# Kernel tuning notes

Measured on AMD Instinct MI355X. Metric: run time of the kernel, lower is better.

## Reference

```python
import jax, jax.numpy as jnp
import numpy as np

S_SRC, S_TGT, N = 50, 50, 64
E, H, V_SRC, V_TGT = 300, 512, 10000, 10000


def setup_inputs() -> dict:
    key = jax.random.key(0)
    ks = jax.random.split(key, 20)
    p = lambda k, shape: jax.random.normal(k, shape, dtype=jnp.float32) * 0.02
    inp = {
        'source': jax.random.randint(ks[0], (S_SRC, N), 0, V_SRC),
        'target': jax.random.randint(ks[1], (S_TGT, N), 0, V_TGT),
        'enc_emb': p(ks[2], (V_SRC, E)),
        'enc_Wih_f': p(ks[3], (4 * H, E)),
        'enc_Whh_f': p(ks[4], (4 * H, H)),
        'enc_b_f': jnp.zeros((4 * H,), jnp.float32),
        'enc_Wih_b': p(ks[5], (4 * H, E)),
        'enc_Whh_b': p(ks[6], (4 * H, H)),
        'enc_b_b': jnp.zeros((4 * H,), jnp.float32),
        'fc_hid_W': p(ks[7], (H, 2 * H)),
        'fc_hid_b': jnp.zeros((H,), jnp.float32),
        'fc_cell_W': p(ks[8], (H, 2 * H)),
        'fc_cell_b': jnp.zeros((H,), jnp.float32),
        'dec_emb': p(ks[9], (V_TGT, E)),
        'dec_Wih': p(ks[10], (4 * H, 2 * H + E)),
        'dec_Whh': p(ks[11], (4 * H, H)),
        'dec_b': jnp.zeros((4 * H,), jnp.float32),
        'energy_W': p(ks[12], (1, 3 * H)),
        'energy_b': jnp.zeros((1,), jnp.float32),
        'fc_W': p(ks[13], (V_TGT, H)),
        'fc_b': jnp.zeros((V_TGT,), jnp.float32),
    }
    return inp


def lstm_cell(x, h, c, Wih, Whh, b):
    # x:[N,Din] h,c:[N,H]  PyTorch gate order: i,f,g,o
    gates = x @ Wih.T + h @ Whh.T + b
    i, f, g, o = jnp.split(gates, 4, axis=-1)
    i, f, o = jax.nn.sigmoid(i), jax.nn.sigmoid(f), jax.nn.sigmoid(o)
    c_new = f * c + i * jnp.tanh(g)
    h_new = o * jnp.tanh(c_new)
    return h_new, c_new


def _forward(source, target, enc_emb, enc_Wih_f, enc_Whh_f, enc_b_f,
             enc_Wih_b, enc_Whh_b, enc_b_b, fc_hid_W, fc_hid_b,
             fc_cell_W, fc_cell_b, dec_emb, dec_Wih, dec_Whh, dec_b,
             energy_W, energy_b, fc_W, fc_b):
    emb = enc_emb[source]  # [S,N,E]  (dropout = identity, eval)
    h0 = jnp.zeros((source.shape[1], H), jnp.float32)

    def fwd_step(carry, x_t):
        h, c = carry
        h, c = lstm_cell(x_t, h, c, enc_Wih_f, enc_Whh_f, enc_b_f)
        return (h, c), h

    def bwd_step(carry, x_t):
        h, c = carry
        h, c = lstm_cell(x_t, h, c, enc_Wih_b, enc_Whh_b, enc_b_b)
        return (h, c), h

    (hf, cf), out_f = jax.lax.scan(fwd_step, (h0, h0), emb)
    (hb, cb), out_b = jax.lax.scan(bwd_step, (h0, h0), emb[::-1])
    encoder_states = jnp.concatenate([out_f, out_b[::-1]], axis=-1)  # [S,N,2H]

    hidden = jnp.concatenate([hf, hb], axis=-1) @ fc_hid_W.T + fc_hid_b  # [N,H]
    cell = jnp.concatenate([cf, cb], axis=-1) @ fc_cell_W.T + fc_cell_b

    def dec_step(carry, x_t):
        h, c = carry
        e = dec_emb[x_t]  # [N,E]
        # energy: Linear(cat(hidden_repeat[S,N,H], enc_states[S,N,2H])) -> [S,N,1]
        Wh, We = energy_W[:, :H], energy_W[:, H:]  # split avoids materializing concat
        energy = jax.nn.relu(h @ Wh.T + jnp.einsum('snl,kl->snk', encoder_states, We) + energy_b)
        attn = jax.nn.softmax(energy, axis=0)  # softmax over seq dim
        context = jnp.einsum('sn,snl->nl', attn[..., 0], encoder_states)  # [N,2H]
        rnn_in = jnp.concatenate([context, e], axis=-1)  # [N,2H+E]
        h, c = lstm_cell(rnn_in, h, c, dec_Wih, dec_Whh, dec_b)
        pred = h @ fc_W.T + fc_b  # [N,V]
        return (h, c), pred

    # teacher_force_ratio=1.0: inputs are target[0..T-2]
    _, preds = jax.lax.scan(dec_step, (hidden, cell), target[:-1])
    zeros0 = jnp.zeros((1,) + preds.shape[1:], preds.dtype)
    return jnp.concatenate([zeros0, preds], axis=0)  # [T,N,V], row 0 zeros


def reference(source, target, enc_emb, enc_Wih_f, enc_Whh_f, enc_b_f,
              enc_Wih_b, enc_Whh_b, enc_b_b, fc_hid_W, fc_hid_b,
              fc_cell_W, fc_cell_b, dec_emb, dec_Wih, dec_Whh, dec_b,
              energy_W, energy_b, fc_W, fc_b):
    return _forward(source, target, enc_emb, enc_Wih_f, enc_Whh_f, enc_b_f,
                    enc_Wih_b, enc_Whh_b, enc_b_b, fc_hid_W, fc_hid_b,
                    fc_cell_W, fc_cell_b, dec_emb, dec_Wih, dec_Whh, dec_b,
                    energy_W, energy_b, fc_W, fc_b)
```

## Files before the change

kernel.cpp:

```cpp
#include <hip/hip_runtime.h>
#include <math.h>

#define SSRC 50
#define NBATCH 64
#define EDIM 300
#define HDIM 512
#define G4H 2048
#define VTGT 10000
#define TSTEPS 49

#define HS4 8192

__device__ __forceinline__ float ld1_agent(const float* p) {
    return __hip_atomic_load(p, __ATOMIC_RELAXED, __HIP_MEMORY_SCOPE_AGENT);
}
__device__ __forceinline__ void st1_agent(float* p, float v) {
    __hip_atomic_store(p, v, __ATOMIC_RELAXED, __HIP_MEMORY_SCOPE_AGENT);
}
__device__ __forceinline__ float2 ld2_agent(const float* p) {
    unsigned long long u = __hip_atomic_load((const unsigned long long*)p,
                                             __ATOMIC_RELAXED, __HIP_MEMORY_SCOPE_AGENT);
    union { unsigned long long u; float2 f; } c; c.u = u; return c.f;
}
__device__ __forceinline__ void st2_agent(float* p, float x, float y) {
    union { float2 f; unsigned long long u; } c; c.f.x = x; c.f.y = y;
    __hip_atomic_store((unsigned long long*)p, c.u, __ATOMIC_RELAXED, __HIP_MEMORY_SCOPE_AGENT);
}

__device__ __forceinline__ void gbar(int* cnt, int nblk, int& gen)
{
    asm volatile("s_waitcnt vmcnt(0)" ::: "memory");
    __syncthreads();
    if (threadIdx.x == 0) {
        __hip_atomic_fetch_add(cnt, 1, __ATOMIC_RELAXED, __HIP_MEMORY_SCOPE_AGENT);
        gen += nblk;
        const long long t0 = (long long)__builtin_amdgcn_s_memrealtime();
        while (__hip_atomic_load(cnt, __ATOMIC_RELAXED, __HIP_MEMORY_SCOPE_AGENT) < gen) {
            __builtin_amdgcn_s_sleep(2);
            if ((long long)__builtin_amdgcn_s_memrealtime() - t0 > 200000000LL) break;
        }
    }
    __syncthreads();
}

__device__ __forceinline__ int gswz(int kk, int c) {
    return kk * 128 + ((c ^ (((c >> 6) & 1) << 2)) ^ (kk << 2));
}

__global__ __launch_bounds__(256)
void gemm_bias_kernel(const float* __restrict__ A, const int* __restrict__ aidx, int lda,
                      const float* __restrict__ B, int ldb,
                      const float* __restrict__ bias,
                      float* __restrict__ C, int ldc,
                      int M, int N, int K, int a_trans)
{
    __shared__ float As[8 * 128];
    __shared__ float Bs[8 * 128];
    const int tid = threadIdx.x;
    const int bm = blockIdx.y * 128;
    const int bn = blockIdx.x * 128;
    const int tx = tid & 15;
    const int ty = tid >> 4;

    float acc[8][8];
#pragma unroll
    for (int i = 0; i < 8; ++i)
#pragma unroll
        for (int j = 0; j < 8; ++j) acc[i][j] = 0.f;

    for (int k0 = 0; k0 < K; k0 += 8) {
#pragma unroll
        for (int i = 0; i < 4; ++i) {
            int idx = tid + i * 256;
            {
                int r, kk;
                if (a_trans) { r = idx & 127; kk = idx >> 7; }
                else         { r = idx >> 3; kk = idx & 7; }
                int gm = bm + r, gk = k0 + kk;
                float va = 0.f;
                if (gm < M && gk < K) {
                    if (a_trans) va = A[(long)gk * lda + gm];
                    else {
                        long arow = aidx ? (long)aidx[gm] : (long)gm;
                        va = A[arow * (long)lda + gk];
                    }
                }
                As[gswz(kk, r)] = va;
            }
            {
                int r = idx >> 3, kk = idx & 7;
                int gn = bn + r, gk = k0 + kk;
                float vb = 0.f;
                if (gn < N && gk < K) vb = B[(long)gn * ldb + gk];
                Bs[gswz(kk, r)] = vb;
            }
        }
        __syncthreads();
#pragma unroll
        for (int kk = 0; kk < 8; ++kk) {
            const float4 a0 = *reinterpret_cast<const float4*>(&As[gswz(kk, ty * 8)]);
            const float4 a1 = *reinterpret_cast<const float4*>(&As[gswz(kk, ty * 8 + 4)]);
            const float4 b0 = *reinterpret_cast<const float4*>(&Bs[gswz(kk, tx * 8)]);
            const float4 b1 = *reinterpret_cast<const float4*>(&Bs[gswz(kk, tx * 8 + 4)]);
            const float a[8] = {a0.x, a0.y, a0.z, a0.w, a1.x, a1.y, a1.z, a1.w};
            const float b[8] = {b0.x, b0.y, b0.z, b0.w, b1.x, b1.y, b1.z, b1.w};
#pragma unroll
            for (int i = 0; i < 8; ++i)
#pragma unroll
                for (int j = 0; j < 8; ++j)
                    acc[i][j] = fmaf(a[i], b[j], acc[i][j]);
        }
        __syncthreads();
    }

#pragma unroll
    for (int i = 0; i < 8; ++i) {
        int m = bm + ty * 8 + i;
        if (m >= M) continue;
#pragma unroll
        for (int j = 0; j < 8; ++j) {
            int n = bn + tx * 8 + j;
            if (n >= N) continue;
            float v = acc[i][j];
            if (bias) v += bias[n];
            C[(long)m * ldc + n] = v;
        }
    }
}

__global__ __launch_bounds__(256)
void enc_wt_kernel(const float* __restrict__ Wf, const float* __restrict__ Wb,
                   float4* __restrict__ Wt)
{
    const int F = blockIdx.x * 256 + threadIdx.x;
    if (F >= 2 * 16 * 128 * 128) return;
    const int jj = F & 127;
    const int l4 = (F >> 7) & 127;
    const int r  = F >> 14;
    const int dir = r >> 4, jg = r & 15;
    const int jglob = (jj & 3) * 512 + jg * 32 + (jj >> 2);
    const float* src = dir ? Wb : Wf;
    Wt[F] = *reinterpret_cast<const float4*>(src + (size_t)jglob * 512 + l4 * 4);
}

__global__ __launch_bounds__(256)
void dec_wt_kernel(const float* __restrict__ Wih, const float* __restrict__ Whh,
                   float4* __restrict__ Wt)
{
    const int F = blockIdx.x * 256 + threadIdx.x;
    if (F >= 32 * 384 * 64) return;
    const int j = F & 63;
    const int t = F >> 6;
    const int l4 = t % 384, jg = t / 384;
    const int jglob = (j & 3) * 512 + jg * 16 + (j >> 2);
    const int l = l4 * 4;
    float4 v;
    if (l < 1024) v = *reinterpret_cast<const float4*>(Wih + (size_t)jglob * 1324 + l);
    else          v = *reinterpret_cast<const float4*>(Whh + (size_t)jglob * 512 + (l - 1024));
    Wt[F] = v;
}

struct EncArgs {
    const float* Xf; const float* Xb;
    const float4* WtE;
    float* hT;
    float* cT;
    float* catSt;
    const float* energy_W; const float* energy_b;
    float* eeT;
    const float* fc_hid_W; const float* fc_hid_b;
    const float* fc_cell_W; const float* fc_cell_b;
    float* dhT;
    float* dcT;
    int* bars;
};

__global__ __launch_bounds__(1024)
void enc_persistent(EncArgs a)
{
    __shared__ float actL[8 * 516];
    __shared__ float red[8 * 8 * 128];
    const int blk = blockIdx.x;
    const int tid = threadIdx.x;
    const int lane = tid & 63;
    const int w    = tid >> 6;
    const int lc   = w >> 1;
    const int jh   = w & 1;
    const int dir  = blk >> 7;
    const int db   = blk & 127;
    const int jg   = (db & 7) * 2 + (db >> 6);
    const int ng   = (db >> 3) & 7;
    int genD = 0, genF = 0;

    const float* X   = dir ? a.Xb : a.Xf;
    float* hTd  = a.hT + (size_t)dir * 2 * 4 * HS4;
    float* cTd  = a.cT + (size_t)dir * 4 * HS4;
    const float4* Wt = a.WtE + (size_t)(dir * 16 + jg) * 128 * 128;

    const int pw_n  = ng * 8 + (tid >> 5);
    const int pw_kl = tid & 31;
    const int pw_k  = jg * 32 + pw_kl;
    const int pw_ci = (pw_k >> 2) * 256 + pw_n * 4 + (pw_k & 3);
    float c_reg = 0.f;

    for (int t = 0; t < SSRC; ++t) {
        const int xoff = dir ? (SSRC - 1 - t) : t;
        const float* hbase = hTd + (size_t)(t & 1) * 4 * HS4;
        float xg0 = 0.f, xg1 = 0.f, xg2 = 0.f, xg3 = 0.f;
        if (tid < 256) {
            const float* Xr = X + (size_t)xoff * (NBATCH * G4H) + pw_n * G4H + pw_k;
            xg0 = __builtin_nontemporal_load(Xr);
            xg1 = __builtin_nontemporal_load(Xr + 512);
            xg2 = __builtin_nontemporal_load(Xr + 1024);
            xg3 = __builtin_nontemporal_load(Xr + 1536);
        }
        {
            const int nh = tid & 7, l4g = tid >> 3;
            const float* hp = hbase + ((size_t)l4g * 64 + ng * 8 + nh) * 4;
            const float2 lo = ld2_agent(hp), hi = ld2_agent(hp + 2);
            float4 v; v.x = lo.x; v.y = lo.y; v.z = hi.x; v.w = hi.y;
            *reinterpret_cast<float4*>(&actL[nh * 516 + l4g * 4]) = v;
        }
        __syncthreads();
        float acc[8];
#pragma unroll
        for (int q = 0; q < 8; ++q) acc[q] = 0.f;
        {
            const float4* wp = Wt + (size_t)(lc * 16) * 128 + jh * 64 + lane;
            for (int i = 0; i < 16; ++i) {
                const float4 wv = wp[(size_t)i * 128];
                const int l4 = lc * 16 + i;
#pragma unroll
                for (int q = 0; q < 8; ++q) {
                    const float4 av = *reinterpret_cast<const float4*>(&actL[q * 516 + l4 * 4]);
                    acc[q] = fmaf(av.w, wv.w, fmaf(av.z, wv.z,
                              fmaf(av.y, wv.y, fmaf(av.x, wv.x, acc[q]))));
                }
            }
        }
#pragma unroll
        for (int q = 0; q < 8; ++q) red[lc * 1024 + q * 128 + jh * 64 + lane] = acc[q];
        __syncthreads();
        if (tid < 256) {
            const int nh = tid >> 5;
            float g0 = xg0, g1 = xg1, g2 = xg2, g3 = xg3;
#pragma unroll
            for (int l2 = 0; l2 < 8; ++l2) {
                const float* rp = &red[l2 * 1024 + nh * 128 + pw_kl * 4];
                g0 += rp[0]; g1 += rp[1]; g2 += rp[2]; g3 += rp[3];
            }
            const float si = 1.f / (1.f + __expf(-g0));
            const float sf = 1.f / (1.f + __expf(-g1));
            const float so = 1.f / (1.f + __expf(-g3));
            const float tg = tanhf(g2);
            c_reg = sf * c_reg + si * tg;
            const float hn = so * tanhf(c_reg);
            st1_agent(&(hTd + (size_t)((t + 1) & 1) * 4 * HS4)[pw_ci], hn);
            st1_agent(&a.catSt[((size_t)xoff * 64 + pw_n) * 1024 + dir * 512 + pw_k], hn);
            if (t == SSRC - 1) st1_agent(&cTd[pw_ci], c_reg);
        }
        gbar(a.bars + dir, 128, genD);
    }
    gbar(a.bars + 2, 256, genF);

    const int n = lane;
    if (blk < SSRC) {
        const int s = blk;
        const int nl = tid & 63, ch = tid >> 6;
        const float* row = a.catSt + ((size_t)s * 64 + nl) * 1024;
        const float* We = a.energy_W + 512;
        float p = 0.f;
        for (int l4 = ch * 16; l4 < ch * 16 + 16; ++l4) {
            const float2 s01 = ld2_agent(row + l4 * 4);
            const float2 s23 = ld2_agent(row + l4 * 4 + 2);
            const float4 wv = *reinterpret_cast<const float4*>(We + l4 * 4);
            p += s01.x * wv.x + s01.y * wv.y + s23.x * wv.z + s23.y * wv.w;
        }
        red[ch * 64 + nl] = p;
        __syncthreads();
        if (ch == 0) {
            float sum = a.energy_b[0];
#pragma unroll
            for (int q = 0; q < 16; ++q) sum += red[q * 64 + nl];
            a.eeT[s * 64 + nl] = sum;
        }
    } else if (blk >= 64 && blk < 192) {
        const bool cell = blk >= 128;
        const int kb2 = (blk & 63) * 8;
        const float* W   = cell ? a.fc_cell_W : a.fc_hid_W;
        const float* bs  = cell ? a.fc_cell_b : a.fc_hid_b;
        const float* Afl = cell ? a.cT : a.hT;
        const float* Abl = cell ? (a.cT + (size_t)4 * HS4) : (a.hT + (size_t)8 * HS4);
        const int kl2 = w >> 1, lh = w & 1;
        const int k = kb2 + kl2;
        const float* Wr = W + (size_t)k * 1024;
        float acc = 0.f;
        for (int l4 = lh * 64; l4 < lh * 64 + 64; ++l4) {
            const float* pA = Afl + ((size_t)l4 * 64 + n) * 4;
            const float2 u01 = ld2_agent(pA), u23 = ld2_agent(pA + 2);
            const float4 wv = *reinterpret_cast<const float4*>(Wr + l4 * 4);
            acc += u01.x * wv.x + u01.y * wv.y + u23.x * wv.z + u23.y * wv.w;
            const float* pB = Abl + ((size_t)l4 * 64 + n) * 4;
            const float2 v01 = ld2_agent(pB), v23 = ld2_agent(pB + 2);
            const float4 wv2 = *reinterpret_cast<const float4*>(Wr + 512 + l4 * 4);
            acc += v01.x * wv2.x + v01.y * wv2.y + v23.x * wv2.z + v23.y * wv2.w;
        }
        red[(kl2 * 2 + lh) * 64 + n] = acc;
        __syncthreads();
        if (w < 8) {
            const float v = bs[kb2 + w] + red[(w * 2) * 64 + n] + red[(w * 2 + 1) * 64 + n];
            const int k2 = kb2 + w;
            const int ci = (k2 >> 2) * 256 + n * 4 + (k2 & 3);
            (cell ? a.dcT : a.dhT)[ci] = v;
        }
    }
}

struct DecArgs {
    const float* Xd;
    const float4* WtD;
    const float* Wh;
    const float* eeT;
    const float* catSt;
    float* dhT;
    const float* dcT;
    float* ctxG;
    float* HsT;
    int* bar;
};

__global__ __launch_bounds__(1024)
void dec_persistent(DecArgs a)
{
    __shared__ float  actL[8][1544];
    __shared__ float  red[16 * 544];
    __shared__ float4 cpart[16][64];
    __shared__ float  WhL[512];
    __shared__ float  eeL[SSRC * 8];
    __shared__ float  attnL[SSRC * 8];
    __shared__ float  hdl[8];
    const int blk = blockIdx.x;
    const int tid = threadIdx.x;
    const int lane = tid & 63;
    const int w    = tid >> 6;
    const int jg   = (blk & 7) * 4 + (blk >> 6);
    const int ng   = (blk >> 3) & 7;
    int gen = 0;
    const float4* Wt = a.WtD + (size_t)jg * 384 * 64;

    if (tid < 512) WhL[tid] = a.Wh[tid];
    if (tid < SSRC * 8) eeL[tid] = a.eeT[(tid >> 3) * 64 + ng * 8 + (tid & 7)];
    __syncthreads();

    const int pw_kl = tid >> 3, pw_nh = tid & 7;
    const int pw_k = jg * 16 + pw_kl;
    const int pw_n = ng * 8 + pw_nh;
    const int pw_ci = (pw_k >> 2) * 256 + pw_n * 4 + (pw_k & 3);
    float c_reg = 0.f;
    if (tid < 128) c_reg = ld1_agent(&a.dcT[pw_ci]);

    for (int t = 0; t < TSTEPS; ++t) {
        const float* hc = a.dhT + (size_t)(t & 1) * 32768;
        float xg0 = 0.f, xg1 = 0.f, xg2 = 0.f, xg3 = 0.f;
        if (tid < 128) {
            const float* Xr = a.Xd + (size_t)t * (NBATCH * G4H) + pw_n * G4H + pw_k;
            xg0 = __builtin_nontemporal_load(Xr);
            xg1 = __builtin_nontemporal_load(Xr + 512);
            xg2 = __builtin_nontemporal_load(Xr + 1024);
            xg3 = __builtin_nontemporal_load(Xr + 1536);
        }
        {
            const int nh = tid & 7, l4g = tid >> 3;
            const float* hp = hc + ((size_t)l4g * 64 + ng * 8 + nh) * 4;
            const float2 lo = ld2_agent(hp), hi = ld2_agent(hp + 2);
            float4 v; v.x = lo.x; v.y = lo.y; v.z = hi.x; v.w = hi.y;
            *reinterpret_cast<float4*>(&actL[nh][1024 + l4g * 4]) = v;
        }
        __syncthreads();
        if (w < 8) {
            const float4 h0 = *reinterpret_cast<const float4*>(&actL[w][1024 + lane * 4]);
            const float4 h1 = *reinterpret_cast<const float4*>(&actL[w][1024 + (lane + 64) * 4]);
            const float4 w0 = *reinterpret_cast<const float4*>(&WhL[lane * 4]);
            const float4 w1 = *reinterpret_cast<const float4*>(&WhL[(lane + 64) * 4]);
            float p = h0.x * w0.x + h0.y * w0.y + h0.z * w0.z + h0.w * w0.w
                    + h1.x * w1.x + h1.y * w1.y + h1.z * w1.z + h1.w * w1.w;
#pragma unroll
            for (int off = 32; off > 0; off >>= 1) p += __shfl_down(p, off);
            if (lane == 0) hdl[w] = p;
        }
        __syncthreads();
        if (tid < 8) {
            const float hd = hdl[tid];
            float m = 0.f;
            for (int s = 0; s < SSRC; ++s) m = fmaxf(m, hd + eeL[s * 8 + tid]);
            float ssum = 0.f;
            for (int s = 0; s < SSRC; ++s) {
                float e = hd + eeL[s * 8 + tid];
                e = e > 0.f ? e : 0.f;
                const float ex = __expf(e - m);
                attnL[s * 8 + tid] = ex;
                ssum += ex;
            }
            const float inv = 1.f / ssum;
            for (int s = 0; s < SSRC; ++s) attnL[s * 8 + tid] *= inv;
        }
        __syncthreads();
        {
            const int sh = tid >> 6, nc = tid & 63;
            const int nh = nc >> 3, c = nc & 7;
            const float* sp = a.catSt + ((size_t)ng * 8 + nh) * 1024 + jg * 32 + c * 4;
            float4 acc4{0.f, 0.f, 0.f, 0.f};
            for (int s = sh; s < SSRC; s += 16) {
                const float aw = attnL[s * 8 + nh];
                const float* q = sp + (size_t)s * 64 * 1024;
                const float2 lo = ld2_agent(q), hi = ld2_agent(q + 2);
                acc4.x = fmaf(aw, lo.x, acc4.x);
                acc4.y = fmaf(aw, lo.y, acc4.y);
                acc4.z = fmaf(aw, hi.x, acc4.z);
                acc4.w = fmaf(aw, hi.y, acc4.w);
            }
            cpart[sh][nc] = acc4;
        }
        __syncthreads();
        if (tid < 64) {
            const int nh = tid >> 3, c = tid & 7;
            float4 s4{0.f, 0.f, 0.f, 0.f};
#pragma unroll
            for (int sh = 0; sh < 16; ++sh) {
                const float4 v = cpart[sh][tid];
                s4.x += v.x; s4.y += v.y; s4.z += v.z; s4.w += v.w;
            }
            float* cp = a.ctxG + ((size_t)ng * 8 + nh) * 1024 + jg * 32 + c * 4;
            st2_agent(cp, s4.x, s4.y);
            st2_agent(cp + 2, s4.z, s4.w);
        }
        gbar(a.bar, 256, gen);
#pragma unroll
        for (int i = 0; i < 2; ++i) {
            const int e = tid + i * 1024;
            const int l4g = e & 255, nh = e >> 8;
            const float* cp = a.ctxG + ((size_t)ng * 8 + nh) * 1024 + l4g * 4;
            const float2 lo = ld2_agent(cp), hi = ld2_agent(cp + 2);
            float4 v; v.x = lo.x; v.y = lo.y; v.z = hi.x; v.w = hi.y;
            *reinterpret_cast<float4*>(&actL[nh][l4g * 4]) = v;
        }
        __syncthreads();
        float acc[8];
#pragma unroll
        for (int q = 0; q < 8; ++q) acc[q] = 0.f;
        {
            const float4* wp = Wt + (size_t)(w * 24) * 64 + lane;
            for (int i = 0; i < 24; ++i) {
                const float4 wv = wp[(size_t)i * 64];
                const int l4 = w * 24 + i;
#pragma unroll
                for (int q = 0; q < 8; ++q) {
                    const float4 av = *reinterpret_cast<const float4*>(&actL[q][l4 * 4]);
                    acc[q] = fmaf(av.w, wv.w, fmaf(av.z, wv.z,
                              fmaf(av.y, wv.y, fmaf(av.x, wv.x, acc[q]))));
                }
            }
        }
#pragma unroll
        for (int q = 0; q < 8; ++q) red[w * 544 + q * 68 + lane] = acc[q];
        __syncthreads();
        if (tid < 128) {
            float g4[4];
#pragma unroll
            for (int g = 0; g < 4; ++g) {
                const int j = pw_kl * 4 + g;
                float v = 0.f;
#pragma unroll
                for (int w2 = 0; w2 < 16; ++w2) v += red[w2 * 544 + pw_nh * 68 + j];
                g4[g] = v;
            }
            g4[0] += xg0; g4[1] += xg1; g4[2] += xg2; g4[3] += xg3;
            const float si = 1.f / (1.f + __expf(-g4[0]));
            const float sf = 1.f / (1.f + __expf(-g4[1]));
            const float so = 1.f / (1.f + __expf(-g4[3]));
            const float tg = tanhf(g4[2]);
            c_reg = sf * c_reg + si * tg;
            const float hn = so * tanhf(c_reg);
            st1_agent(&(a.dhT + (size_t)((t + 1) & 1) * 32768)[pw_ci], hn);
            st1_agent(&a.HsT[(size_t)pw_k * (TSTEPS * NBATCH) + t * 64 + pw_n], hn);
        }
        gbar(a.bar, 256, gen);
    }
}

extern "C" void kernel_launch(void* const* d_in, const int* in_sizes, int n_in,
                              void* d_out, int out_size, void* d_ws, size_t ws_size,
                              hipStream_t stream)
{
    const int*   source    = (const int*)  d_in[0];
    const int*   target    = (const int*)  d_in[1];
    const float* enc_emb   = (const float*)d_in[2];
    const float* enc_Wih_f = (const float*)d_in[3];
    const float* enc_Whh_f = (const float*)d_in[4];
    const float* enc_b_f   = (const float*)d_in[5];
    const float* enc_Wih_b = (const float*)d_in[6];
    const float* enc_Whh_b = (const float*)d_in[7];
    const float* enc_b_b   = (const float*)d_in[8];
    const float* fc_hid_W  = (const float*)d_in[9];
    const float* fc_hid_b  = (const float*)d_in[10];
    const float* fc_cell_W = (const float*)d_in[11];
    const float* fc_cell_b = (const float*)d_in[12];
    const float* dec_emb   = (const float*)d_in[13];
    const float* dec_Wih   = (const float*)d_in[14];
    const float* dec_Whh   = (const float*)d_in[15];
    const float* dec_b     = (const float*)d_in[16];
    const float* energy_W  = (const float*)d_in[17];
    const float* energy_b  = (const float*)d_in[18];
    const float* fc_W      = (const float*)d_in[19];
    const float* fc_b      = (const float*)d_in[20];
    float* out = (float*)d_out;

    float* w = (float*)d_ws;
    size_t o = 0;
    auto alloc = [&](size_t nf) { float* p = w + o; o += nf; return p; };
    const size_t HS = (size_t)NBATCH * HDIM;
    float* Xf    = alloc((size_t)SSRC * NBATCH * G4H);
    float* Xb    = alloc((size_t)SSRC * NBATCH * G4H);
    float* catSt = alloc((size_t)SSRC * NBATCH * 1024);
    float* hT    = alloc(4 * HS);
    float* cT    = alloc(2 * HS);
    float* dhT   = alloc(2 * HS);
    float* dcT   = alloc(1 * HS);
    float* eeT   = alloc((size_t)SSRC * NBATCH);
    float* HsT   = alloc((size_t)HDIM * TSTEPS * NBATCH);
    float* WtE   = alloc((size_t)2 * 16 * 128 * 512);
    int*   bars  = (int*)alloc(16);
    float* Xd    = Xf;
    float* ctxG  = hT;
    float* WtD   = Xb;

    hipMemsetAsync(hT, 0, 4 * HS * sizeof(float), stream);
    hipMemsetAsync(bars, 0, 16 * sizeof(int), stream);
    hipMemsetAsync(out, 0, (size_t)NBATCH * VTGT * sizeof(float), stream);

    {
        dim3 g(G4H / 128, (SSRC * NBATCH + 127) / 128);
        gemm_bias_kernel<<<g, 256, 0, stream>>>(enc_emb, source, EDIM, enc_Wih_f, EDIM,
                                                enc_b_f, Xf, G4H, SSRC * NBATCH, G4H, EDIM, 0);
        gemm_bias_kernel<<<g, 256, 0, stream>>>(enc_emb, source, EDIM, enc_Wih_b, EDIM,
                                                enc_b_b, Xb, G4H, SSRC * NBATCH, G4H, EDIM, 0);
    }
    enc_wt_kernel<<<(2 * 16 * 128 * 128 + 255) / 256, 256, 0, stream>>>(
        enc_Whh_f, enc_Whh_b, (float4*)WtE);

    {
        EncArgs ea{Xf, Xb, (const float4*)WtE, hT, cT, catSt,
                   energy_W, energy_b, eeT, fc_hid_W, fc_hid_b, fc_cell_W, fc_cell_b,
                   dhT, dcT, bars};
        enc_persistent<<<256, 1024, 0, stream>>>(ea);
    }

    {
        dim3 g(G4H / 128, (TSTEPS * NBATCH + 127) / 128);
        gemm_bias_kernel<<<g, 256, 0, stream>>>(dec_emb, target, EDIM, dec_Wih + 2 * HDIM,
                                                2 * HDIM + EDIM, dec_b, Xd, G4H,
                                                TSTEPS * NBATCH, G4H, EDIM, 0);
    }
    dec_wt_kernel<<<(32 * 384 * 64 + 255) / 256, 256, 0, stream>>>(
        dec_Wih, dec_Whh, (float4*)WtD);

    {
        DecArgs da{Xd, (const float4*)WtD, energy_W, eeT, catSt,
                   dhT, dcT, ctxG, HsT, bars + 3};
        dec_persistent<<<256, 1024, 0, stream>>>(da);
    }

    {
        dim3 g((VTGT + 127) / 128, (TSTEPS * NBATCH + 127) / 128);
        gemm_bias_kernel<<<g, 256, 0, stream>>>(HsT, nullptr, TSTEPS * NBATCH, fc_W, HDIM,
                                                fc_b, out + (size_t)NBATCH * VTGT, VTGT,
                                                TSTEPS * NBATCH, VTGT, HDIM, 1);
    }
}
```

Before: 3.800 ms.

## Precompute attention-context gate projection and remove mid-step grid barrier in decoder

Uses linearity to precompute Wih_ctx · encoder_states for every source position (a GEMM over all 50 positions before the decoder). The per-step context term then becomes an attention-weighted sum of these precomputed gate contributions, which removes the ctxG exchange and one grid barrier per step and shrinks the recurrent matvec to the Whh part only. The attention dot product h·Wh is also computed as per-block partials written at the end of the previous step. The trade-off is a large up-front GEMM plus extra reads of G4 each step.

```diff
diff --git a/kernel.cpp b/kernel.cpp
--- a/kernel.cpp
+++ b/kernel.cpp
@@ -21,10 +21,6 @@
     unsigned long long u = __hip_atomic_load((const unsigned long long*)p,
                                              __ATOMIC_RELAXED, __HIP_MEMORY_SCOPE_AGENT);
     union { unsigned long long u; float2 f; } c; c.u = u; return c.f;
-}
-__device__ __forceinline__ void st2_agent(float* p, float x, float y) {
-    union { float2 f; unsigned long long u; } c; c.f.x = x; c.f.y = y;
-    __hip_atomic_store((unsigned long long*)p, c.u, __ATOMIC_RELAXED, __HIP_MEMORY_SCOPE_AGENT);
 }
 
 __device__ __forceinline__ void gbar(int* cnt, int nblk, int& gen)
@@ -52,7 +48,7 @@
                       const float* __restrict__ B, int ldb,
                       const float* __restrict__ bias,
                       float* __restrict__ C, int ldc,
-                      int M, int N, int K, int a_trans)
+                      int M, int N, int K, int a_trans, int c_mode)
 {
     __shared__ float As[8 * 128];
     __shared__ float Bs[8 * 128];
@@ -123,7 +119,13 @@
             if (n >= N) continue;
             float v = acc[i][j];
             if (bias) v += bias[n];
-            C[(long)m * ldc + n] = v;
+            if (c_mode == 0) {
+                C[(long)m * ldc + n] = v;
+            } else {
+                const int jg = m >> 6, jl = m & 63;
+                const int s = n >> 6, ng = (n >> 3) & 7, nl = n & 7;
+                C[(size_t)(((jg * 8 + ng) * 50 + s) * 512) + jl * 8 + nl] = v;
+            }
         }
     }
 }
@@ -144,20 +146,23 @@
 }
 
 __global__ __launch_bounds__(256)
-void dec_wt_kernel(const float* __restrict__ Wih, const float* __restrict__ Whh,
-                   float4* __restrict__ Wt)
+void dec_wt3_kernel(const float* __restrict__ Whh, float4* __restrict__ Wt)
 {
     const int F = blockIdx.x * 256 + threadIdx.x;
-    if (F >= 32 * 384 * 64) return;
-    const int j = F & 63;
-    const int t = F >> 6;
-    const int l4 = t % 384, jg = t / 384;
+    if (F >= 32 * 128 * 64) return;
+    const int j  = F & 63;
+    const int l4 = (F >> 6) & 127;
+    const int jg = F >> 13;
     const int jglob = (j & 3) * 512 + jg * 16 + (j >> 2);
-    const int l = l4 * 4;
-    float4 v;
-    if (l < 1024) v = *reinterpret_cast<const float4*>(Wih + (size_t)jglob * 1324 + l);
-    else          v = *reinterpret_cast<const float4*>(Whh + (size_t)jglob * 512 + (l - 1024));
-    Wt[F] = v;
+    Wt[F] = *reinterpret_cast<const float4*>(Whh + (size_t)jglob * 512 + l4 * 4);
+}
+
+__global__ __launch_bounds__(256)
+void aidx_kernel(int* __restrict__ aidx)
+{
+    const int m = blockIdx.x * 256 + threadIdx.x;
+    if (m >= 2048) return;
+    aidx[m] = (m & 3) * 512 + (m >> 6) * 16 + ((m >> 2) & 15);
 }
 
 struct EncArgs {
@@ -318,13 +323,13 @@
 
 struct DecArgs {
     const float* Xd;
-    const float4* WtD;
+    const float4* Wt3;
+    const float* G4;
     const float* Wh;
     const float* eeT;
-    const float* catSt;
     float* dhT;
     const float* dcT;
-    float* ctxG;
+    float* hdP;
     float* HsT;
     int* bar;
 };
@@ -332,24 +337,27 @@
 __global__ __launch_bounds__(1024)
 void dec_persistent(DecArgs a)
 {
-    __shared__ float  actL[8][1544];
+    __shared__ float  actL[8][520];
     __shared__ float  red[16 * 544];
-    __shared__ float4 cpart[16][64];
+    __shared__ float4 red3[8][64][2];
     __shared__ float  WhL[512];
-    __shared__ float  eeL[SSRC * 8];
-    __shared__ float  attnL[SSRC * 8];
+    __shared__ float  eeL[SSRC][9];
+    __shared__ float  attnL[SSRC][8];
     __shared__ float  hdl[8];
+    __shared__ float  hdpl[32][8];
+    __shared__ float  hdkl[16][8];
     const int blk = blockIdx.x;
     const int tid = threadIdx.x;
-    const int lane = tid & 63;
-    const int w    = tid >> 6;
-    const int jg   = (blk & 7) * 4 + (blk >> 6);
-    const int ng   = (blk >> 3) & 7;
+    const int lane = tid & 63, w = tid >> 6;
+    const int jg = (blk & 7) * 4 + ((blk >> 3) & 3);
+    const int ng = blk >> 5;
     int gen = 0;
-    const float4* Wt = a.WtD + (size_t)jg * 384 * 64;
+    const float4* Wt = a.Wt3 + (size_t)jg * 128 * 64;
+    const float*  Gt = a.G4 + (size_t)(jg * 8 + ng) * 50 * 512;
 
     if (tid < 512) WhL[tid] = a.Wh[tid];
-    if (tid < SSRC * 8) eeL[tid] = a.eeT[(tid >> 3) * 64 + ng * 8 + (tid & 7)];
+    if (tid < SSRC * 8)
+        eeL[tid >> 3][tid & 7] = a.eeT[(tid >> 3) * 64 + ng * 8 + (tid & 7)];
     __syncthreads();
 
     const int pw_kl = tid >> 3, pw_nh = tid & 7;
@@ -361,6 +369,13 @@
 
     for (int t = 0; t < TSTEPS; ++t) {
         const float* hc = a.dhT + (size_t)(t & 1) * 32768;
+        {
+            const int nh = tid & 7, l4g = tid >> 3;
+            const float* hp = hc + ((size_t)l4g * 64 + ng * 8 + nh) * 4;
+            const float2 lo = ld2_agent(hp), hi = ld2_agent(hp + 2);
+            float4 v; v.x = lo.x; v.y = lo.y; v.z = hi.x; v.w = hi.y;
+            *reinterpret_cast<float4*>(&actL[nh][l4g * 4]) = v;
+        }
         float xg0 = 0.f, xg1 = 0.f, xg2 = 0.f, xg3 = 0.f;
         if (tid < 128) {
             const float* Xr = a.Xd + (size_t)t * (NBATCH * G4H) + pw_n * G4H + pw_k;
@@ -369,112 +384,95 @@
             xg2 = __builtin_nontemporal_load(Xr + 1024);
             xg3 = __builtin_nontemporal_load(Xr + 1536);
         }
+        __syncthreads();
+        if (t == 0) {
+            if (w < 8) {
+                const float4 h0 = *reinterpret_cast<const float4*>(&actL[w][lane * 4]);
+                const float4 h1 = *reinterpret_cast<const float4*>(&actL[w][(lane + 64) * 4]);
+                const float4 w0 = *reinterpret_cast<const float4*>(&WhL[lane * 4]);
+                const float4 w1 = *reinterpret_cast<const float4*>(&WhL[(lane + 64) * 4]);
+                float p = h0.x * w0.x + h0.y * w0.y + h0.z * w0.z + h0.w * w0.w
+                        + h1.x * w1.x + h1.y * w1.y + h1.z * w1.z + h1.w * w1.w;
+#pragma unroll
+                for (int off = 32; off > 0; off >>= 1) p += __shfl_down(p, off);
+                if (lane == 0) hdl[w] = p;
+            }
+        } else {
+            if (tid < 256) {
+                const int q = tid >> 3, nh = tid & 7;
+                hdpl[q][nh] = ld1_agent(&a.hdP[q * 64 + ng * 8 + nh]);
+            }
+            __syncthreads();
+            if (tid < 8) {
+                float s = 0.f;
+#pragma unroll
+                for (int q = 0; q < 32; ++q) s += hdpl[q][tid];
+                hdl[tid] = s;
+            }
+        }
+        __syncthreads();
+        if (w < 8) {
+            const float hd = hdl[w];
+            float e = 0.f;
+            if (lane < SSRC) { e = hd + eeL[lane][w]; e = e > 0.f ? e : 0.f; }
+            float m = e;
+#pragma unroll
+            for (int off = 32; off > 0; off >>= 1) m = fmaxf(m, __shfl_xor(m, off));
+            float ex = (lane < SSRC) ? __expf(e - m) : 0.f;
+            float ssum = ex;
+#pragma unroll
+            for (int off = 32; off > 0; off >>= 1) ssum += __shfl_xor(ssum, off);
+            if (lane < SSRC) attnL[lane][w] = ex / ssum;
+        }
+        __syncthreads();
         {
-            const int nh = tid & 7, l4g = tid >> 3;
-            const float* hp = hc + ((size_t)l4g * 64 + ng * 8 + nh) * 4;
-            const float2 lo = ld2_agent(hp), hi = ld2_agent(hp + 2);
-            float4 v; v.x = lo.x; v.y = lo.y; v.z = hi.x; v.w = hi.y;
-            *reinterpret_cast<float4*>(&actL[nh][1024 + l4g * 4]) = v;
-        }
-        __syncthreads();
-        if (w < 8) {
-            const float4 h0 = *reinterpret_cast<const float4*>(&actL[w][1024 + lane * 4]);
-            const float4 h1 = *reinterpret_cast<const float4*>(&actL[w][1024 + (lane + 64) * 4]);
-            const float4 w0 = *reinterpret_cast<const float4*>(&WhL[lane * 4]);
-            const float4 w1 = *reinterpret_cast<const float4*>(&WhL[(lane + 64) * 4]);
-            float p = h0.x * w0.x + h0.y * w0.y + h0.z * w0.z + h0.w * w0.w
-                    + h1.x * w1.x + h1.y * w1.y + h1.z * w1.z + h1.w * w1.w;
-#pragma unroll
-            for (int off = 32; off > 0; off >>= 1) p += __shfl_down(p, off);
-            if (lane == 0) hdl[w] = p;
-        }
-        __syncthreads();
-        if (tid < 8) {
-            const float hd = hdl[tid];
-            float m = 0.f;
-            for (int s = 0; s < SSRC; ++s) m = fmaxf(m, hd + eeL[s * 8 + tid]);
-            float ssum = 0.f;
-            for (int s = 0; s < SSRC; ++s) {
-                float e = hd + eeL[s * 8 + tid];
-                e = e > 0.f ? e : 0.f;
-                const float ex = __expf(e - m);
-                attnL[s * 8 + tid] = ex;
-                ssum += ex;
-            }
-            const float inv = 1.f / ssum;
-            for (int s = 0; s < SSRC; ++s) attnL[s * 8 + tid] *= inv;
-        }
-        __syncthreads();
+            const int jl = tid & 63, sh = (tid >> 6) & 7, nhh = tid >> 9;
+            const float* Gp = Gt + jl * 8 + nhh * 4;
+            float4 acc4{0.f, 0.f, 0.f, 0.f};
+            for (int s = sh; s < SSRC; s += 8) {
+                const float4 av = *reinterpret_cast<const float4*>(&attnL[s][nhh * 4]);
+                const float4 gv = *reinterpret_cast<const float4*>(Gp + (size_t)s * 512);
+                acc4.x = fmaf(av.x, gv.x, acc4.x);
+                acc4.y = fmaf(av.y, gv.y, acc4.y);
+                acc4.z = fmaf(av.z, gv.z, acc4.z);
+                acc4.w = fmaf(av.w, gv.w, acc4.w);
+            }
+            red3[sh][jl][nhh] = acc4;
+        }
         {
-            const int sh = tid >> 6, nc = tid & 63;
-            const int nh = nc >> 3, c = nc & 7;
-            const float* sp = a.catSt + ((size_t)ng * 8 + nh) * 1024 + jg * 32 + c * 4;
-            float4 acc4{0.f, 0.f, 0.f, 0.f};
-            for (int s = sh; s < SSRC; s += 16) {
-                const float aw = attnL[s * 8 + nh];
-                const float* q = sp + (size_t)s * 64 * 1024;
-                const float2 lo = ld2_agent(q), hi = ld2_agent(q + 2);
-                acc4.x = fmaf(aw, lo.x, acc4.x);
-                acc4.y = fmaf(aw, lo.y, acc4.y);
-                acc4.z = fmaf(aw, hi.x, acc4.z);
-                acc4.w = fmaf(aw, hi.y, acc4.w);
-            }
-            cpart[sh][nc] = acc4;
-        }
-        __syncthreads();
-        if (tid < 64) {
-            const int nh = tid >> 3, c = tid & 7;
-            float4 s4{0.f, 0.f, 0.f, 0.f};
-#pragma unroll
-            for (int sh = 0; sh < 16; ++sh) {
-                const float4 v = cpart[sh][tid];
-                s4.x += v.x; s4.y += v.y; s4.z += v.z; s4.w += v.w;
-            }
-            float* cp = a.ctxG + ((size_t)ng * 8 + nh) * 1024 + jg * 32 + c * 4;
-            st2_agent(cp, s4.x, s4.y);
-            st2_agent(cp + 2, s4.z, s4.w);
-        }
-        gbar(a.bar, 256, gen);
-#pragma unroll
-        for (int i = 0; i < 2; ++i) {
-            const int e = tid + i * 1024;
-            const int l4g = e & 255, nh = e >> 8;
-            const float* cp = a.ctxG + ((size_t)ng * 8 + nh) * 1024 + l4g * 4;
-            const float2 lo = ld2_agent(cp), hi = ld2_agent(cp + 2);
-            float4 v; v.x = lo.x; v.y = lo.y; v.z = hi.x; v.w = hi.y;
-            *reinterpret_cast<float4*>(&actL[nh][l4g * 4]) = v;
-        }
-        __syncthreads();
-        float acc[8];
-#pragma unroll
-        for (int q = 0; q < 8; ++q) acc[q] = 0.f;
-        {
-            const float4* wp = Wt + (size_t)(w * 24) * 64 + lane;
-            for (int i = 0; i < 24; ++i) {
+            float acc2[8];
+#pragma unroll
+            for (int q = 0; q < 8; ++q) acc2[q] = 0.f;
+            const float4* wp = Wt + (size_t)(w * 8) * 64 + lane;
+            for (int i = 0; i < 8; ++i) {
                 const float4 wv = wp[(size_t)i * 64];
-                const int l4 = w * 24 + i;
+                const int l4 = w * 8 + i;
 #pragma unroll
                 for (int q = 0; q < 8; ++q) {
                     const float4 av = *reinterpret_cast<const float4*>(&actL[q][l4 * 4]);
-                    acc[q] = fmaf(av.w, wv.w, fmaf(av.z, wv.z,
-                              fmaf(av.y, wv.y, fmaf(av.x, wv.x, acc[q]))));
+                    acc2[q] = fmaf(av.w, wv.w, fmaf(av.z, wv.z,
+                               fmaf(av.y, wv.y, fmaf(av.x, wv.x, acc2[q]))));
                 }
             }
-        }
-#pragma unroll
-        for (int q = 0; q < 8; ++q) red[w * 544 + q * 68 + lane] = acc[q];
+#pragma unroll
+            for (int q = 0; q < 8; ++q) red[w * 544 + q * 68 + lane] = acc2[q];
+        }
         __syncthreads();
         if (tid < 128) {
-            float g4[4];
+            const float* r3f = reinterpret_cast<const float*>(red3);
+            const int base = pw_nh >> 2, cc = pw_nh & 3;
+            float g4[4] = {xg0, xg1, xg2, xg3};
 #pragma unroll
             for (int g = 0; g < 4; ++g) {
                 const int j = pw_kl * 4 + g;
-                float v = 0.f;
+                float v = g4[g];
 #pragma unroll
                 for (int w2 = 0; w2 < 16; ++w2) v += red[w2 * 544 + pw_nh * 68 + j];
+#pragma unroll
+                for (int sh = 0; sh < 8; ++sh)
+                    v += r3f[(size_t)(sh * 128 + j * 2 + base) * 4 + cc];
                 g4[g] = v;
             }
-            g4[0] += xg0; g4[1] += xg1; g4[2] += xg2; g4[3] += xg3;
             const float si = 1.f / (1.f + __expf(-g4[0]));
             const float sf = 1.f / (1.f + __expf(-g4[1]));
             const float so = 1.f / (1.f + __expf(-g4[3]));
@@ -483,6 +481,14 @@
             const float hn = so * tanhf(c_reg);
             st1_agent(&(a.dhT + (size_t)((t + 1) & 1) * 32768)[pw_ci], hn);
             st1_agent(&a.HsT[(size_t)pw_k * (TSTEPS * NBATCH) + t * 64 + pw_n], hn);
+            hdkl[pw_kl][pw_nh] = WhL[pw_k] * hn;
+        }
+        __syncthreads();
+        if (tid < 8) {
+            float s = 0.f;
+#pragma unroll
+            for (int kl = 0; kl < 16; ++kl) s += hdkl[kl][tid];
+            st1_agent(&a.hdP[jg * 64 + ng * 8 + tid], s);
         }
         gbar(a.bar, 256, gen);
     }
@@ -529,10 +535,12 @@
     float* eeT   = alloc((size_t)SSRC * NBATCH);
     float* HsT   = alloc((size_t)HDIM * TSTEPS * NBATCH);
     float* WtE   = alloc((size_t)2 * 16 * 128 * 512);
+    float* Wt3   = alloc((size_t)32 * 128 * 64 * 4);
+    float* hdP   = alloc((size_t)32 * 64);
+    int*   aidxA = (int*)alloc(2048);
     int*   bars  = (int*)alloc(16);
     float* Xd    = Xf;
-    float* ctxG  = hT;
-    float* WtD   = Xb;
+    float* G4    = Xb;
 
     hipMemsetAsync(hT, 0, 4 * HS * sizeof(float), stream);
     hipMemsetAsync(bars, 0, 16 * sizeof(int), stream);
@@ -541,12 +549,13 @@
     {
         dim3 g(G4H / 128, (SSRC * NBATCH + 127) / 128);
         gemm_bias_kernel<<<g, 256, 0, stream>>>(enc_emb, source, EDIM, enc_Wih_f, EDIM,
-                                                enc_b_f, Xf, G4H, SSRC * NBATCH, G4H, EDIM, 0);
+                                                enc_b_f, Xf, G4H, SSRC * NBATCH, G4H, EDIM, 0, 0);
         gemm_bias_kernel<<<g, 256, 0, stream>>>(enc_emb, source, EDIM, enc_Wih_b, EDIM,
-                                                enc_b_b, Xb, G4H, SSRC * NBATCH, G4H, EDIM, 0);
+                                                enc_b_b, Xb, G4H, SSRC * NBATCH, G4H, EDIM, 0, 0);
     }
     enc_wt_kernel<<<(2 * 16 * 128 * 128 + 255) / 256, 256, 0, stream>>>(
         enc_Whh_f, enc_Whh_b, (float4*)WtE);
+    aidx_kernel<<<8, 256, 0, stream>>>(aidxA);
 
     {
         EncArgs ea{Xf, Xb, (const float4*)WtE, hT, cT, catSt,
@@ -559,14 +568,19 @@
         dim3 g(G4H / 128, (TSTEPS * NBATCH + 127) / 128);
         gemm_bias_kernel<<<g, 256, 0, stream>>>(dec_emb, target, EDIM, dec_Wih + 2 * HDIM,
                                                 2 * HDIM + EDIM, dec_b, Xd, G4H,
-                                                TSTEPS * NBATCH, G4H, EDIM, 0);
-    }
-    dec_wt_kernel<<<(32 * 384 * 64 + 255) / 256, 256, 0, stream>>>(
-        dec_Wih, dec_Whh, (float4*)WtD);
-
+                                                TSTEPS * NBATCH, G4H, EDIM, 0, 0);
+    }
     {
-        DecArgs da{Xd, (const float4*)WtD, energy_W, eeT, catSt,
-                   dhT, dcT, ctxG, HsT, bars + 3};
+        dim3 g(3200 / 128, 2048 / 128);
+        gemm_bias_kernel<<<g, 256, 0, stream>>>(dec_Wih, aidxA, 2 * HDIM + EDIM,
+                                                catSt, 1024, nullptr,
+                                                G4, 3200, 2048, 3200, 1024, 0, 1);
+    }
+    dec_wt3_kernel<<<(32 * 128 * 64 + 255) / 256, 256, 0, stream>>>(dec_Whh, (float4*)Wt3);
+
+    {
+        DecArgs da{Xd, (const float4*)Wt3, G4, energy_W, eeT,
+                   dhT, dcT, hdP, HsT, bars + 3};
         dec_persistent<<<256, 1024, 0, stream>>>(da);
     }
 
@@ -574,6 +588,6 @@
         dim3 g((VTGT + 127) / 128, (TSTEPS * NBATCH + 127) / 128);
         gemm_bias_kernel<<<g, 256, 0, stream>>>(HsT, nullptr, TSTEPS * NBATCH, fc_W, HDIM,
                                                 fc_b, out + (size_t)NBATCH * VTGT, VTGT,
-                                                TSTEPS * NBATCH, VTGT, HDIM, 1);
-    }
-}
+                                                TSTEPS * NBATCH, VTGT, HDIM, 1, 0);
+    }
+}
```

Measured after the change: 3.452 ms. 9.1% less time.
